# Optimization experiments

Hardware: AMD Instinct MI355X
Metric: run time of the kernel (lower is better)

The kernel has to match this reference:

```python
import jax, jax.numpy as jnp
import numpy as np

B, S, D, H, K = 2, 4096, 256, 8, 32  # batch, seq, d_model, heads, key_dim
LN_EPS = 1e-3  # keras LayerNormalization default epsilon
NEG_INF = -1e9


def setup_inputs() -> dict:
    key = jax.random.key(0)
    ks = jax.random.split(key, 12)
    sd = 1.0 / np.sqrt(D)
    inp = {
        "x": jax.random.normal(ks[0], (B, S, D), dtype=jnp.float32),
        "Wq": jax.random.normal(ks[1], (D, H, K), dtype=jnp.float32) * sd,
        "bq": jnp.zeros((H, K), dtype=jnp.float32),
        "Wk": jax.random.normal(ks[2], (D, H, K), dtype=jnp.float32) * sd,
        "bk": jnp.zeros((H, K), dtype=jnp.float32),
        "Wv": jax.random.normal(ks[3], (D, H, K), dtype=jnp.float32) * sd,
        "bv": jnp.zeros((H, K), dtype=jnp.float32),
        "Wo": jax.random.normal(ks[4], (H, K, D), dtype=jnp.float32) * (1.0 / np.sqrt(H * K)),
        "bo": jnp.zeros((D,), dtype=jnp.float32),
        "gamma": jnp.ones((D,), dtype=jnp.float32),
        "beta": jnp.zeros((D,), dtype=jnp.float32),
        "w_2": 64,
    }
    return inp


def reference(x, Wq, bq, Wk, bk, Wv, bv, Wo, bo, gamma, beta, w_2):
    # q/k/v projections: [B,S,D] -> [B,S,H,K]
    q = jnp.einsum("bsd,dhk->bshk", x, Wq) + bq
    k = jnp.einsum("bsd,dhk->bshk", x, Wk) + bk
    v = jnp.einsum("bsd,dhk->bshk", x, Wv) + bv

    # dense scores (keras MHA computes full L^2 then masks): [B,H,S,S]
    scores = jnp.einsum("bqhk,bshk->bhqs", q, k) / jnp.sqrt(jnp.float32(K))

    # sliding-window band mask |i-j| <= w_2, applied additively like keras
    i = jnp.arange(S)
    band = (jnp.abs(i[:, None] - i[None, :]) <= w_2)  # [S,S]
    scores = scores + (1.0 - band.astype(scores.dtype)) * NEG_INF

    attn = jax.nn.softmax(scores, axis=-1)
    o = jnp.einsum("bhqs,bshk->bqhk", attn, v)
    attn_out = jnp.einsum("bqhk,hkd->bqd", o, Wo) + bo

    # residual add + LayerNorm (last axis)
    y = x + attn_out
    mu = jnp.mean(y, axis=-1, keepdims=True)
    var = jnp.mean(jnp.square(y - mu), axis=-1, keepdims=True)
    return (y - mu) * jax.lax.rsqrt(var + LN_EPS) * gamma + beta
```

## Files before the change

### kernel.cpp

```cpp
#include <hip/hip_runtime.h>
#include <hip/hip_bf16.h>
#include <cmath>

constexpr int B = 2, S = 4096, D = 256, H = 8, K = 32;
constexpr int HK = H * K;
constexpr float LN_EPS = 1e-3f;

constexpr int QT  = 64;
constexpr int WIN = 192;
constexpr int VSTRIDE = 4224;

typedef short bf16x8 __attribute__((ext_vector_type(8)));
typedef float f32x4  __attribute__((ext_vector_type(4)));

static __device__ inline short f2bf(float f) {
    unsigned u = __float_as_uint(f);
    unsigned r = (u + 0x7fffu + ((u >> 16) & 1u)) >> 16;
    return (short)r;
}

static __device__ inline int frag_off(int row, int q) {
    return ((row << 2) + (q ^ ((row >> 1) & 3))) << 4;
}

__global__ __launch_bounds__(256) void wcvt_kernel(
    const float* __restrict__ Wq, const float* __restrict__ Wk,
    const float* __restrict__ Wv, const float* __restrict__ Wo,
    const float* __restrict__ x,
    short* __restrict__ wqt, short* __restrict__ wkt,
    short* __restrict__ wvt, short* __restrict__ wot,
    short* __restrict__ vtb, short* __restrict__ xb)
{
    const int t = threadIdx.x;
    if (blockIdx.x >= 32) {
        const int i = ((blockIdx.x - 32) * 256 + t) * 8;
        const float4 a = *(const float4*)(x + i);
        const float4 b = *(const float4*)(x + i + 4);
        bf16x8 o;
        o[0] = f2bf(a.x); o[1] = f2bf(a.y); o[2] = f2bf(a.z); o[3] = f2bf(a.w);
        o[4] = f2bf(b.x); o[5] = f2bf(b.y); o[6] = f2bf(b.z); o[7] = f2bf(b.w);
        *(bf16x8*)(xb + i) = o;
        return;
    }
    const int mat = blockIdx.x >> 3, strip = blockIdx.x & 7;
    const int d0 = strip * 32;
    const float* src = (mat == 0) ? Wq : (mat == 1) ? Wk : (mat == 2) ? Wv : Wo;
    short* dst = (mat == 0) ? wqt : (mat == 1) ? wkt : (mat == 2) ? wvt : wot;

    __shared__ float lds[32][257];
    {
        const int row = t >> 3, c0 = (t & 7) * 32;
#pragma unroll
        for (int i = 0; i < 8; ++i) {
            const float4 f = *(const float4*)(src + (size_t)(d0 + row) * 256 + c0 + i * 4);
            lds[row][c0 + i * 4 + 0] = f.x; lds[row][c0 + i * 4 + 1] = f.y;
            lds[row][c0 + i * 4 + 2] = f.z; lds[row][c0 + i * 4 + 3] = f.w;
        }
    }
    __syncthreads();
    short* orow = dst + (size_t)t * 256 + d0;
#pragma unroll
    for (int u = 0; u < 4; ++u) {
        bf16x8 v;
#pragma unroll
        for (int j = 0; j < 8; ++j)
            v[j] = f2bf(lds[u * 8 + j][t]);
        *(bf16x8*)(orow + u * 8) = v;
    }

    {
        const int e0 = (blockIdx.x * 256 + t) * 8;
        const int r = e0 >> 7;
        const int c = e0 & 127;
        const int col = (c < 64) ? c : (VSTRIDE - 128 + c);
        short* p = vtb + (size_t)r * VSTRIDE + col;
#pragma unroll
        for (int j = 0; j < 8; ++j) p[j] = 0;
    }
}

__global__ __launch_bounds__(256) void qkv_gemm_kernel(
    const short* __restrict__ xb,
    const short* __restrict__ wqt, const short* __restrict__ wkt,
    const short* __restrict__ wvt,
    const float* __restrict__ bq, const float* __restrict__ bk,
    const float* __restrict__ bv,
    short* __restrict__ qb, short* __restrict__ kb, short* __restrict__ vtb)
{
    const int nt = blockIdx.x % 6, mt = blockIdx.x / 6;
    const int mat = nt >> 1, n0 = (nt & 1) * 128, m0 = mt * 64;
    const short* wt  = (mat == 0) ? wqt : (mat == 1) ? wkt : wvt;
    const float* bia = (mat == 0) ? bq  : (mat == 1) ? bk  : bv;

    __shared__ alignas(16) char lds[24576];
    char* AsB = lds;
    char* BsB = lds + 8192;

    const int t = threadIdx.x, wave = t >> 6, lane = t & 63;
    const int quad = lane >> 4, l16 = lane & 15;
    const int wm = (wave & 1) * 32, wn = (wave >> 1) * 64;

    int arow[2], auk[2], brow[4], buk[4];
#pragma unroll
    for (int i = 0; i < 2; ++i) {
        const int idx = t * 2 + i;
        arow[i] = idx >> 3; auk[i] = idx & 7;
    }
#pragma unroll
    for (int i = 0; i < 4; ++i) {
        const int idx = t * 4 + i;
        brow[i] = idx >> 3; buk[i] = idx & 7;
    }

    f32x4 acc[2][4];
#pragma unroll
    for (int i = 0; i < 2; ++i)
#pragma unroll
        for (int j = 0; j < 4; ++j) acc[i][j] = (f32x4){0.f, 0.f, 0.f, 0.f};

    bf16x8 an[2], bn[4];
#pragma unroll
    for (int i = 0; i < 2; ++i)
        an[i] = *(const bf16x8*)(xb + (size_t)(m0 + arow[i]) * 256 + auk[i] * 8);
#pragma unroll
    for (int i = 0; i < 4; ++i)
        bn[i] = *(const bf16x8*)(wt + (size_t)(n0 + brow[i]) * 256 + buk[i] * 8);

    for (int kk = 0; kk < 4; ++kk) {
        __syncthreads();
#pragma unroll
        for (int i = 0; i < 2; ++i)
            *(bf16x8*)(AsB + (auk[i] >> 2) * 4096 + frag_off(arow[i], auk[i] & 3)) = an[i];
#pragma unroll
        for (int i = 0; i < 4; ++i)
            *(bf16x8*)(BsB + (buk[i] >> 2) * 8192 + frag_off(brow[i], buk[i] & 3)) = bn[i];
        __syncthreads();
        if (kk < 3) {
            const int kc = (kk + 1) * 64;
#pragma unroll
            for (int i = 0; i < 2; ++i)
                an[i] = *(const bf16x8*)(xb + (size_t)(m0 + arow[i]) * 256 + kc + auk[i] * 8);
#pragma unroll
            for (int i = 0; i < 4; ++i)
                bn[i] = *(const bf16x8*)(wt + (size_t)(n0 + brow[i]) * 256 + kc + buk[i] * 8);
        }
#pragma unroll
        for (int hh = 0; hh < 2; ++hh) {
            bf16x8 af[2], bf[4];
#pragma unroll
            for (int mi = 0; mi < 2; ++mi)
                af[mi] = *(const bf16x8*)(AsB + hh * 4096 + frag_off(wm + mi * 16 + l16, quad));
#pragma unroll
            for (int ni = 0; ni < 4; ++ni)
                bf[ni] = *(const bf16x8*)(BsB + hh * 8192 + frag_off(wn + ni * 16 + l16, quad));
#pragma unroll
            for (int mi = 0; mi < 2; ++mi)
#pragma unroll
                for (int ni = 0; ni < 4; ++ni)
                    acc[mi][ni] = __builtin_amdgcn_mfma_f32_16x16x32_bf16(
                        af[mi], bf[ni], acc[mi][ni], 0, 0, 0);
        }
    }

    if (mat < 2) {
        short* dst = (mat == 0) ? qb : kb;
#pragma unroll
        for (int ni = 0; ni < 4; ++ni) {
            const int gn = n0 + wn + ni * 16 + l16;
            const float bb = bia[gn];
            const int h = gn >> 5, k2 = gn & 31;
#pragma unroll
            for (int mi = 0; mi < 2; ++mi)
#pragma unroll
                for (int r = 0; r < 4; ++r) {
                    const int gm = m0 + wm + mi * 16 + quad * 4 + r;
                    const int b = gm >> 12, s = gm & 4095;
                    dst[(((size_t)(b * 8 + h)) * 4096 + s) * 32 + k2] = f2bf(acc[mi][ni][r] + bb);
                }
        }
    } else {
#pragma unroll
        for (int ni = 0; ni < 4; ++ni) {
            const int gn = n0 + wn + ni * 16 + l16;
            const float bb = bia[gn];
            const int h = gn >> 5, k2 = gn & 31;
#pragma unroll
            for (int mi = 0; mi < 2; ++mi) {
                const int gm0 = m0 + wm + mi * 16 + quad * 4;
                const int b = gm0 >> 12, s0 = gm0 & 4095;
                short4 pk;
                pk.x = f2bf(acc[mi][ni][0] + bb);
                pk.y = f2bf(acc[mi][ni][1] + bb);
                pk.z = f2bf(acc[mi][ni][2] + bb);
                pk.w = f2bf(acc[mi][ni][3] + bb);
                *(short4*)(vtb + ((size_t)(b * 8 + h) * 32 + k2) * VSTRIDE + 64 + s0) = pk;
            }
        }
    }
}

__global__ __launch_bounds__(256) void attn_kernel(
    const short* __restrict__ qb, const short* __restrict__ kb,
    const short* __restrict__ vtb, short* __restrict__ ob,
    const int* __restrict__ w2p)
{
    const int w2 = *w2p;
    const int bh   = blockIdx.x >> 6;
    const int tile = blockIdx.x & 63;
    const int i0 = tile * QT, jlo = i0 - w2;
    const int t = threadIdx.x, wave = t >> 6, lane = t & 63;
    const int quad = lane >> 4, l16 = lane & 15;

    __shared__ alignas(16) char lds[38912];
    short* Vts = (short*)lds;
    short* Ps  = (short*)(lds + 13312);

#pragma unroll
    for (int it = 0; it < 3; ++it) {
        const int idx = t + it * 256;
        const int row = idx / 24, unit = idx % 24;
        *(bf16x8*)(Vts + row * 200 + unit * 8) =
            *(const bf16x8*)(vtb + ((size_t)bh * 32 + row) * VSTRIDE + (jlo + 64) + unit * 8);
    }
    if (t < 192) Vts[32 * 200 + t] = (short)0x3F80;

    bf16x8 af[4];
#pragma unroll
    for (int mi = 0; mi < 4; ++mi)
        af[mi] = *(const bf16x8*)(qb + ((size_t)bh * 4096 + i0 + mi * 16 + l16) * 32 + quad * 8);

    f32x4 sc[4][3];
#pragma unroll
    for (int mi = 0; mi < 4; ++mi)
#pragma unroll
        for (int ni = 0; ni < 3; ++ni) sc[mi][ni] = (f32x4){0.f, 0.f, 0.f, 0.f};
#pragma unroll
    for (int ni = 0; ni < 3; ++ni) {
        const int krow = wave * 48 + ni * 16 + l16;
        const int jc = min(max(jlo + krow, 0), S - 1);
        const bf16x8 bfr = *(const bf16x8*)(kb + ((size_t)bh * 4096 + jc) * 32 + quad * 8);
#pragma unroll
        for (int mi = 0; mi < 4; ++mi)
            sc[mi][ni] = __builtin_amdgcn_mfma_f32_16x16x32_bf16(af[mi], bfr, sc[mi][ni], 0, 0, 0);
    }

    const float scale = 0.17677669529663687f;
    int colv[3]; bool jok[3];
#pragma unroll
    for (int ni = 0; ni < 3; ++ni) {
        colv[ni] = wave * 48 + ni * 16 + l16;
        const int j = jlo + colv[ni];
        jok[ni] = (j >= 0) && (j < S);
    }
#pragma unroll
    for (int mi = 0; mi < 4; ++mi)
#pragma unroll
        for (int r = 0; r < 4; ++r) {
            const int row = mi * 16 + quad * 4 + r;
#pragma unroll
            for (int ni = 0; ni < 3; ++ni) {
                const int diff = colv[ni] - row;
                const bool valid = jok[ni] && (diff >= 0) && (diff <= 2 * w2);
                const float p = valid ? __expf(sc[mi][ni][r] * scale) : 0.f;
                Ps[row * 200 + colv[ni]] = f2bf(p);
            }
        }
    __syncthreads();

    const int orow0 = wave * 16;
    f32x4 oacc[3];
#pragma unroll
    for (int ni = 0; ni < 3; ++ni) oacc[ni] = (f32x4){0.f, 0.f, 0.f, 0.f};
#pragma unroll
    for (int kk = 0; kk < 6; ++kk) {
        const bf16x8 pa = *(const bf16x8*)(Ps + (orow0 + l16) * 200 + kk * 32 + quad * 8);
#pragma unroll
        for (int ni = 0; ni < 3; ++ni) {
            const bf16x8 vb = *(const bf16x8*)(Vts + (ni * 16 + l16) * 200 + kk * 32 + quad * 8);
            oacc[ni] = __builtin_amdgcn_mfma_f32_16x16x32_bf16(pa, vb, oacc[ni], 0, 0, 0);
        }
    }

    const int b = bh >> 3, h = bh & 7;
#pragma unroll
    for (int r = 0; r < 4; ++r) {
        const int row = orow0 + quad * 4 + r;
        const float L = __shfl(oacc[2][r], lane & 48);
        const float Linv = 1.f / L;
        const int s = i0 + row;
#pragma unroll
        for (int ni = 0; ni < 2; ++ni) {
            const int d = ni * 16 + l16;
            ob[((size_t)b * 4096 + s) * 256 + h * 32 + d] = f2bf(oacc[ni][r] * Linv);
        }
    }
}

__global__ __launch_bounds__(256) void out_ln_kernel(
    const short* __restrict__ o, const short* __restrict__ wot,
    const float* __restrict__ x, const float* __restrict__ bo,
    const float* __restrict__ gamma, const float* __restrict__ beta,
    float* __restrict__ out)
{
    __shared__ float ys[16][260];

    const int t = threadIdx.x, wave = t >> 6, lane = t & 63;
    const int quad = lane >> 4, l16 = lane & 15;
    const int m0 = blockIdx.x * 16;
    const int wn = wave * 64;

    const short* abase = o   + (size_t)(m0 + l16) * 256 + quad * 8;
    const short* bbase = wot + (size_t)(wn + l16) * 256 + quad * 8;

    f32x4 acc[4];
#pragma unroll
    for (int j = 0; j < 4; ++j) acc[j] = (f32x4){0.f, 0.f, 0.f, 0.f};

#pragma unroll 2
    for (int k0 = 0; k0 < 256; k0 += 32) {
        const bf16x8 af = *(const bf16x8*)(abase + k0);
        bf16x8 bf[4];
#pragma unroll
        for (int ni = 0; ni < 4; ++ni)
            bf[ni] = *(const bf16x8*)(bbase + (size_t)ni * 16 * 256 + k0);
#pragma unroll
        for (int ni = 0; ni < 4; ++ni)
            acc[ni] = __builtin_amdgcn_mfma_f32_16x16x32_bf16(af, bf[ni], acc[ni], 0, 0, 0);
    }

#pragma unroll
    for (int ni = 0; ni < 4; ++ni) {
        const float bov = bo[wn + ni * 16 + l16];
#pragma unroll
        for (int r = 0; r < 4; ++r)
            ys[quad * 4 + r][wn + ni * 16 + l16] = acc[ni][r] + bov;
    }
    __syncthreads();

    const float4 g4 = *(const float4*)(gamma + lane * 4);
    const float4 b4 = *(const float4*)(beta + lane * 4);
#pragma unroll
    for (int rr = 0; rr < 4; ++rr) {
        const int row = wave * 4 + rr;
        const float4 av = *(const float4*)(&ys[row][lane * 4]);
        const float4 xv = *(const float4*)(x + (size_t)(m0 + row) * 256 + lane * 4);
        const float y0 = xv.x + av.x, y1 = xv.y + av.y, y2 = xv.z + av.z, y3 = xv.w + av.w;
        float sum = y0 + y1 + y2 + y3;
        float s2 = y0 * y0 + y1 * y1 + y2 * y2 + y3 * y3;
#pragma unroll
        for (int off = 32; off > 0; off >>= 1) {
            sum += __shfl_xor(sum, off);
            s2 += __shfl_xor(s2, off);
        }
        const float mu = sum * (1.f / 256.f);
        const float rstd = rsqrtf(s2 * (1.f / 256.f) - mu * mu + LN_EPS);
        float4 ov;
        ov.x = (y0 - mu) * rstd * g4.x + b4.x;
        ov.y = (y1 - mu) * rstd * g4.y + b4.y;
        ov.z = (y2 - mu) * rstd * g4.z + b4.z;
        ov.w = (y3 - mu) * rstd * g4.w + b4.w;
        *(float4*)(out + (size_t)(m0 + row) * 256 + lane * 4) = ov;
    }
}

extern "C" void kernel_launch(void* const* d_in, const int* in_sizes, int n_in,
                              void* d_out, int out_size, void* d_ws, size_t ws_size,
                              hipStream_t stream) {
    const float* x     = (const float*)d_in[0];
    const float* Wq    = (const float*)d_in[1];
    const float* bq    = (const float*)d_in[2];
    const float* Wk    = (const float*)d_in[3];
    const float* bk    = (const float*)d_in[4];
    const float* Wv    = (const float*)d_in[5];
    const float* bv    = (const float*)d_in[6];
    const float* Wo    = (const float*)d_in[7];
    const float* bo    = (const float*)d_in[8];
    const float* gamma = (const float*)d_in[9];
    const float* beta  = (const float*)d_in[10];
    const int*   w2p   = (const int*)d_in[11];
    float* out = (float*)d_out;

    const size_t NQ = (size_t)B * H * S * K;
    short* qb  = (short*)d_ws;
    short* kb  = qb + NQ;
    short* vtb = kb + NQ;
    short* ob  = vtb + (size_t)16 * 32 * VSTRIDE;
    short* wqt = ob + NQ;
    short* wkt = wqt + 65536;
    short* wvt = wkt + 65536;
    short* wot = wvt + 65536;
    short* xb  = wot + 65536;

    wcvt_kernel<<<dim3(32 + 1024), dim3(256), 0, stream>>>(
        Wq, Wk, Wv, Wo, x, wqt, wkt, wvt, wot, vtb, xb);

    qkv_gemm_kernel<<<dim3(768), dim3(256), 0, stream>>>(
        xb, wqt, wkt, wvt, bq, bk, bv, qb, kb, vtb);

    attn_kernel<<<dim3(B * H * S / QT), dim3(256), 0, stream>>>(
        qb, kb, vtb, ob, w2p);

    out_ln_kernel<<<dim3(B * S / 16), dim3(256), 0, stream>>>(
        ob, wot, x, bo, gamma, beta, out);
}
```

Baseline: 117.4 us.

## Fuse x bf16 conversion into QKV GEMM and halve its M tile

The fp32 input x is no longer converted to a bf16 buffer in the weight-conversion kernel. The QKV GEMM now loads fp32 x directly and rounds it to bf16 while staging the tile in LDS. The GEMM M tile shrinks from 64 to 32 rows, so the grid doubles to 1536 blocks and each wave computes a single 16-row MFMA fragment. This removes a full write and re-read of the bf16 x buffer and most of the conversion kernel's blocks, at the cost of reading twice as many bytes of x per GEMM block and less reuse of the weight tiles.

After: 120.5 us. 2.7% more time.

```diff
diff --git a/kernel.cpp b/kernel.cpp
--- a/kernel.cpp
+++ b/kernel.cpp
@@ -26,22 +26,11 @@
 __global__ __launch_bounds__(256) void wcvt_kernel(
     const float* __restrict__ Wq, const float* __restrict__ Wk,
     const float* __restrict__ Wv, const float* __restrict__ Wo,
-    const float* __restrict__ x,
     short* __restrict__ wqt, short* __restrict__ wkt,
     short* __restrict__ wvt, short* __restrict__ wot,
-    short* __restrict__ vtb, short* __restrict__ xb)
+    short* __restrict__ vtb)
 {
     const int t = threadIdx.x;
-    if (blockIdx.x >= 32) {
-        const int i = ((blockIdx.x - 32) * 256 + t) * 8;
-        const float4 a = *(const float4*)(x + i);
-        const float4 b = *(const float4*)(x + i + 4);
-        bf16x8 o;
-        o[0] = f2bf(a.x); o[1] = f2bf(a.y); o[2] = f2bf(a.z); o[3] = f2bf(a.w);
-        o[4] = f2bf(b.x); o[5] = f2bf(b.y); o[6] = f2bf(b.z); o[7] = f2bf(b.w);
-        *(bf16x8*)(xb + i) = o;
-        return;
-    }
     const int mat = blockIdx.x >> 3, strip = blockIdx.x & 7;
     const int d0 = strip * 32;
     const float* src = (mat == 0) ? Wq : (mat == 1) ? Wk : (mat == 2) ? Wv : Wo;
@@ -80,7 +69,7 @@
 }
 
 __global__ __launch_bounds__(256) void qkv_gemm_kernel(
-    const short* __restrict__ xb,
+    const float* __restrict__ x,
     const short* __restrict__ wqt, const short* __restrict__ wkt,
     const short* __restrict__ wvt,
     const float* __restrict__ bq, const float* __restrict__ bk,
@@ -88,77 +77,70 @@
     short* __restrict__ qb, short* __restrict__ kb, short* __restrict__ vtb)
 {
     const int nt = blockIdx.x % 6, mt = blockIdx.x / 6;
-    const int mat = nt >> 1, n0 = (nt & 1) * 128, m0 = mt * 64;
+    const int mat = nt >> 1, n0 = (nt & 1) * 128, m0 = mt * 32;
     const short* wt  = (mat == 0) ? wqt : (mat == 1) ? wkt : wvt;
     const float* bia = (mat == 0) ? bq  : (mat == 1) ? bk  : bv;
 
-    __shared__ alignas(16) char lds[24576];
+    __shared__ alignas(16) char lds[20480];
     char* AsB = lds;
-    char* BsB = lds + 8192;
+    char* BsB = lds + 4096;
 
     const int t = threadIdx.x, wave = t >> 6, lane = t & 63;
     const int quad = lane >> 4, l16 = lane & 15;
-    const int wm = (wave & 1) * 32, wn = (wave >> 1) * 64;
-
-    int arow[2], auk[2], brow[4], buk[4];
-#pragma unroll
-    for (int i = 0; i < 2; ++i) {
-        const int idx = t * 2 + i;
-        arow[i] = idx >> 3; auk[i] = idx & 7;
-    }
+    const int wm = (wave & 1) * 16, wn = (wave >> 1) * 64;
+
+    const int arow = t >> 3, auk = t & 7;
+    int brow[4], buk[4];
 #pragma unroll
     for (int i = 0; i < 4; ++i) {
         const int idx = t * 4 + i;
         brow[i] = idx >> 3; buk[i] = idx & 7;
     }
 
-    f32x4 acc[2][4];
-#pragma unroll
-    for (int i = 0; i < 2; ++i)
-#pragma unroll
-        for (int j = 0; j < 4; ++j) acc[i][j] = (f32x4){0.f, 0.f, 0.f, 0.f};
-
-    bf16x8 an[2], bn[4];
-#pragma unroll
-    for (int i = 0; i < 2; ++i)
-        an[i] = *(const bf16x8*)(xb + (size_t)(m0 + arow[i]) * 256 + auk[i] * 8);
+    const float* xrow = x + (size_t)(m0 + arow) * 256 + auk * 8;
+
+    f32x4 acc[4];
+#pragma unroll
+    for (int j = 0; j < 4; ++j) acc[j] = (f32x4){0.f, 0.f, 0.f, 0.f};
+
+    float4 ax0, ax1;
+    bf16x8 bn[4];
+    ax0 = *(const float4*)(xrow);
+    ax1 = *(const float4*)(xrow + 4);
 #pragma unroll
     for (int i = 0; i < 4; ++i)
         bn[i] = *(const bf16x8*)(wt + (size_t)(n0 + brow[i]) * 256 + buk[i] * 8);
 
     for (int kk = 0; kk < 4; ++kk) {
         __syncthreads();
-#pragma unroll
-        for (int i = 0; i < 2; ++i)
-            *(bf16x8*)(AsB + (auk[i] >> 2) * 4096 + frag_off(arow[i], auk[i] & 3)) = an[i];
+        {
+            bf16x8 av;
+            av[0] = f2bf(ax0.x); av[1] = f2bf(ax0.y); av[2] = f2bf(ax0.z); av[3] = f2bf(ax0.w);
+            av[4] = f2bf(ax1.x); av[5] = f2bf(ax1.y); av[6] = f2bf(ax1.z); av[7] = f2bf(ax1.w);
+            *(bf16x8*)(AsB + (auk >> 2) * 2048 + frag_off(arow, auk & 3)) = av;
+        }
 #pragma unroll
         for (int i = 0; i < 4; ++i)
             *(bf16x8*)(BsB + (buk[i] >> 2) * 8192 + frag_off(brow[i], buk[i] & 3)) = bn[i];
         __syncthreads();
         if (kk < 3) {
             const int kc = (kk + 1) * 64;
-#pragma unroll
-            for (int i = 0; i < 2; ++i)
-                an[i] = *(const bf16x8*)(xb + (size_t)(m0 + arow[i]) * 256 + kc + auk[i] * 8);
+            ax0 = *(const float4*)(xrow + kc);
+            ax1 = *(const float4*)(xrow + kc + 4);
 #pragma unroll
             for (int i = 0; i < 4; ++i)
                 bn[i] = *(const bf16x8*)(wt + (size_t)(n0 + brow[i]) * 256 + kc + buk[i] * 8);
         }
 #pragma unroll
         for (int hh = 0; hh < 2; ++hh) {
-            bf16x8 af[2], bf[4];
-#pragma unroll
-            for (int mi = 0; mi < 2; ++mi)
-                af[mi] = *(const bf16x8*)(AsB + hh * 4096 + frag_off(wm + mi * 16 + l16, quad));
+            const bf16x8 af = *(const bf16x8*)(AsB + hh * 2048 + frag_off(wm + l16, quad));
+            bf16x8 bf[4];
 #pragma unroll
             for (int ni = 0; ni < 4; ++ni)
                 bf[ni] = *(const bf16x8*)(BsB + hh * 8192 + frag_off(wn + ni * 16 + l16, quad));
 #pragma unroll
-            for (int mi = 0; mi < 2; ++mi)
-#pragma unroll
-                for (int ni = 0; ni < 4; ++ni)
-                    acc[mi][ni] = __builtin_amdgcn_mfma_f32_16x16x32_bf16(
-                        af[mi], bf[ni], acc[mi][ni], 0, 0, 0);
+            for (int ni = 0; ni < 4; ++ni)
+                acc[ni] = __builtin_amdgcn_mfma_f32_16x16x32_bf16(af, bf[ni], acc[ni], 0, 0, 0);
         }
     }
 
@@ -170,13 +152,11 @@
             const float bb = bia[gn];
             const int h = gn >> 5, k2 = gn & 31;
 #pragma unroll
-            for (int mi = 0; mi < 2; ++mi)
-#pragma unroll
-                for (int r = 0; r < 4; ++r) {
-                    const int gm = m0 + wm + mi * 16 + quad * 4 + r;
-                    const int b = gm >> 12, s = gm & 4095;
-                    dst[(((size_t)(b * 8 + h)) * 4096 + s) * 32 + k2] = f2bf(acc[mi][ni][r] + bb);
-                }
+            for (int r = 0; r < 4; ++r) {
+                const int gm = m0 + wm + quad * 4 + r;
+                const int b = gm >> 12, s = gm & 4095;
+                dst[(((size_t)(b * 8 + h)) * 4096 + s) * 32 + k2] = f2bf(acc[ni][r] + bb);
+            }
         }
     } else {
 #pragma unroll
@@ -184,17 +164,14 @@
             const int gn = n0 + wn + ni * 16 + l16;
             const float bb = bia[gn];
             const int h = gn >> 5, k2 = gn & 31;
-#pragma unroll
-            for (int mi = 0; mi < 2; ++mi) {
-                const int gm0 = m0 + wm + mi * 16 + quad * 4;
-                const int b = gm0 >> 12, s0 = gm0 & 4095;
-                short4 pk;
-                pk.x = f2bf(acc[mi][ni][0] + bb);
-                pk.y = f2bf(acc[mi][ni][1] + bb);
-                pk.z = f2bf(acc[mi][ni][2] + bb);
-                pk.w = f2bf(acc[mi][ni][3] + bb);
-                *(short4*)(vtb + ((size_t)(b * 8 + h) * 32 + k2) * VSTRIDE + 64 + s0) = pk;
-            }
+            const int gm0 = m0 + wm + quad * 4;
+            const int b = gm0 >> 12, s0 = gm0 & 4095;
+            short4 pk;
+            pk.x = f2bf(acc[ni][0] + bb);
+            pk.y = f2bf(acc[ni][1] + bb);
+            pk.z = f2bf(acc[ni][2] + bb);
+            pk.w = f2bf(acc[ni][3] + bb);
+            *(short4*)(vtb + ((size_t)(b * 8 + h) * 32 + k2) * VSTRIDE + 64 + s0) = pk;
         }
     }
 }
@@ -389,13 +366,12 @@
     short* wkt = wqt + 65536;
     short* wvt = wkt + 65536;
     short* wot = wvt + 65536;
-    short* xb  = wot + 65536;
-
-    wcvt_kernel<<<dim3(32 + 1024), dim3(256), 0, stream>>>(
-        Wq, Wk, Wv, Wo, x, wqt, wkt, wvt, wot, vtb, xb);
-
-    qkv_gemm_kernel<<<dim3(768), dim3(256), 0, stream>>>(
-        xb, wqt, wkt, wvt, bq, bk, bv, qb, kb, vtb);
+
+    wcvt_kernel<<<dim3(32), dim3(256), 0, stream>>>(
+        Wq, Wk, Wv, Wo, wqt, wkt, wvt, wot, vtb);
+
+    qkv_gemm_kernel<<<dim3(1536), dim3(256), 0, stream>>>(
+        x, wqt, wkt, wvt, bq, bk, bv, qb, kb, vtb);
 
     attn_kernel<<<dim3(B * H * S / QT), dim3(256), 0, stream>>>(
         qb, kb, vtb, ob, w2p);
```
